# Optimization experiments

Measured on AMD Instinct MI355X. Metric: run time of the kernel, lower is better.

Reference implementation:

```python
import jax, jax.numpy as jnp
import numpy as np

B, C, H, W = 8, 768, 64, 64
BOT = 64   # bottleneck_dim
PD = 96    # prompt_dim
KP = 32    # number of prompt tokens
KK = 9     # 3x3 kernel points


def gelu(x):
    return jax.nn.gelu(x, approximate=False)  # torch nn.GELU default (erf)


def layernorm(x, g, b, eps=1e-5):
    m = jnp.mean(x, axis=-1, keepdims=True)
    v = jnp.var(x, axis=-1, keepdims=True)
    return (x - m) * jax.lax.rsqrt(v + eps) * g + b


def conv3x3(x, w, b):
    # x [B,Ci,H,W], w [Co,Ci,3,3] (torch layout), stride 1, pad 1
    y = jax.lax.conv_general_dilated(x, w, (1, 1), ((1, 1), (1, 1)))
    return y + b[None, :, None, None]


def deform_conv3x3(x, offset, w, pad=1):
    # mmcv DeformConv2d (v1, no mask, bias=False), deform_groups=1.
    # x [B,Ci,H,W]; offset [B,2*KK,H,W] in (dy,dx) pairs per kernel point.
    Bn, Ci, Hn, Wn = x.shape
    Co = w.shape[0]
    off = offset.reshape(Bn, KK, 2, Hn, Wn)
    dy, dx = off[:, :, 0], off[:, :, 1]                      # [B,KK,H,W]
    ky, kx = jnp.meshgrid(jnp.arange(3), jnp.arange(3), indexing='ij')
    py = (jnp.arange(Hn, dtype=x.dtype)[None, None, :, None] - pad
          + ky.reshape(1, KK, 1, 1).astype(x.dtype) + dy)    # sample rows
    px = (jnp.arange(Wn, dtype=x.dtype)[None, None, None, :] - pad
          + kx.reshape(1, KK, 1, 1).astype(x.dtype) + dx)    # sample cols
    y0 = jnp.floor(py)
    x0 = jnp.floor(px)
    wy = (py - y0)[:, None]                                   # [B,1,KK,H,W]
    wx = (px - x0)[:, None]
    xf = x.reshape(Bn, Ci, Hn * Wn)
    y0i = y0.astype(jnp.int32)
    x0i = x0.astype(jnp.int32)

    def samp(yi, xi):
        valid = ((yi >= 0) & (yi < Hn) & (xi >= 0) & (xi < Wn))
        yc = jnp.clip(yi, 0, Hn - 1)
        xc = jnp.clip(xi, 0, Wn - 1)
        idx = (yc * Wn + xc).reshape(Bn, -1)                  # [B,KK*H*W]
        g = jax.vmap(lambda f, i: f[:, i])(xf, idx)           # [B,Ci,KK*H*W]
        g = g.reshape(Bn, Ci, KK, Hn, Wn)
        return g * valid[:, None].astype(x.dtype)

    g00 = samp(y0i, x0i)
    g01 = samp(y0i, x0i + 1)
    g10 = samp(y0i + 1, x0i)
    g11 = samp(y0i + 1, x0i + 1)
    val = (g00 * (1 - wy) * (1 - wx) + g01 * (1 - wy) * wx
           + g10 * wy * (1 - wx) + g11 * wy * wx)             # [B,Ci,KK,H,W]
    return jnp.einsum('bckhw,ock->bohw', val, w.reshape(Co, Ci, KK))


def setup_inputs() -> dict:
    key = jax.random.key(0)
    ks = jax.random.split(key, 16)
    s = 0.02
    inp = {
        'x': jax.random.normal(ks[0], (B, C, H, W), jnp.float32),
        'irf': jax.random.normal(ks[1], (B, BOT, H, W), jnp.float32),
        'tf': jax.random.normal(ks[2], (KP, PD), jnp.float32),
        'ln_g': jnp.ones((C,), jnp.float32),
        'ln_b': jnp.zeros((C,), jnp.float32),
        'Wd': jax.random.normal(ks[3], (C, BOT), jnp.float32) * s,
        'bd': jnp.zeros((BOT,), jnp.float32),
        'Wu': jax.random.normal(ks[4], (BOT, C), jnp.float32) * s,
        'bu': jnp.zeros((C,), jnp.float32),
        'off_w': jax.random.normal(ks[5], (2 * KK, 2 * BOT, 3, 3), jnp.float32) * s,
        'off_b': jnp.zeros((2 * KK,), jnp.float32),
        'mod_w1': jax.random.normal(ks[6], (BOT // 4, BOT), jnp.float32) * s,
        'mod_b1': jnp.zeros((BOT // 4,), jnp.float32),
        'mod_w2': jax.random.normal(ks[7], (BOT, BOT // 4), jnp.float32) * s,
        'mod_b2': jnp.zeros((BOT,), jnp.float32),
        'dc_w': jax.random.normal(ks[8], (BOT, BOT, 3, 3), jnp.float32) * s,
        'alpha': jnp.full((1,), 0.1, jnp.float32),
        'Wk': jax.random.normal(ks[9], (PD, C), jnp.float32) * s,
        'bk': jnp.zeros((C,), jnp.float32),
        'Wv': jax.random.normal(ks[10], (PD, C), jnp.float32) * s,
        'bv': jnp.zeros((C,), jnp.float32),
        'temperature': jnp.full((1,), 0.07, jnp.float32),
        'Wg1': jax.random.normal(ks[11], (C, C // 4), jnp.float32) * s,
        'bg1': jnp.zeros((C // 4,), jnp.float32),
        'Wg2': jax.random.normal(ks[12], (C // 4, 1), jnp.float32) * s,
        'bg2': jnp.zeros((1,), jnp.float32),
        'scale': jnp.full((1,), 0.1, jnp.float32),
    }
    return inp


def reference(x, irf, tf, ln_g, ln_b, Wd, bd, Wu, bu, off_w, off_b,
              mod_w1, mod_b1, mod_w2, mod_b2, dc_w, alpha,
              Wk, bk, Wv, bv, temperature, Wg1, bg1, Wg2, bg2, scale):
    identity = x
    xp = jnp.transpose(x, (0, 2, 3, 1))                       # [B,H,W,C]
    x_down = gelu(layernorm(xp, ln_g, ln_b) @ Wd + bd)        # [B,H,W,BOT]
    # --- IRRGBFuse ---
    xc = jnp.transpose(x_down, (0, 3, 1, 2))                  # [B,BOT,H,W]
    offset = conv3x3(jnp.concatenate([xc, irf], axis=1), off_w, off_b)
    x_def = deform_conv3x3(xc, offset, dc_w)                  # [B,BOT,H,W]
    m = jnp.einsum('bchw,oc->bohw', irf, mod_w1) + mod_b1[None, :, None, None]
    m = jnp.einsum('bchw,oc->bohw', gelu(m), mod_w2) + mod_b2[None, :, None, None]
    m = jax.nn.sigmoid(m)
    x_fused = x_def + alpha * (x_def * m)
    x_fused = jnp.transpose(x_fused, (0, 2, 3, 1))            # [B,H,W,BOT]
    # --- up-projection + residual (dropout inactive in eval) ---
    x_up = x_fused @ Wu + bu
    x_res1 = xp + scale * x_up                                # [B,H,W,C]
    x_flat = x_res1.reshape(B, H * W, C)
    # --- cosine cross-attention over prompts ---
    pk = tf @ Wk + bk                                          # [K,C]
    pv = tf @ Wv + bv
    xn = x_flat / jnp.maximum(jnp.linalg.norm(x_flat, axis=-1, keepdims=True), 1e-12)
    pkn = pk / jnp.maximum(jnp.linalg.norm(pk, axis=-1, keepdims=True), 1e-12)
    cos = jnp.einsum('bnc,kc->bnk', xn, pkn)
    attn = jax.nn.softmax(cos / temperature, axis=-1)
    x_prompted = jnp.einsum('bnk,kc->bnc', attn, pv).reshape(B, H, W, C)
    # --- gate + residuals ---
    g = jax.nn.sigmoid(gelu(x_res1 @ Wg1 + bg1) @ Wg2 + bg2)   # [B,H,W,1]
    x_gated = x_res1 + g * x_prompted
    return identity + scale * jnp.transpose(x_gated, (0, 3, 1, 2))
```

## Files before the change

kernel.cpp:

```cpp
#include <hip/hip_runtime.h>
#include <hip/hip_bf16.h>
#include <math.h>

#define BN 8
#define C 768
#define H 64
#define W 64
#define HW 4096
#define BOT 64
#define PD 96
#define KP 32
#define KKN 9
#define NPX (BN*HW)

typedef __hip_bfloat16 bf16;
typedef __attribute__((ext_vector_type(8))) short bf16x8;
typedef __attribute__((ext_vector_type(4))) float f32x4;
#define MFMA16(a,b,c) __builtin_amdgcn_mfma_f32_16x16x32_bf16(a,b,c,0,0,0)

__device__ __forceinline__ float gelu_f(float x) {
    return 0.5f * x * (1.0f + erff(x * 0.70710678118654752440f));
}
__device__ __forceinline__ float sigmoid_f(float x) {
    return 1.0f / (1.0f + __expf(-x));
}
__device__ __forceinline__ float bf2f(short s) {
    return __uint_as_float(((unsigned)(unsigned short)s) << 16);
}

__global__ void k_prep(const float* __restrict__ Wd, const float* __restrict__ ln_g,
                       const float* __restrict__ ln_b, const float* __restrict__ bd,
                       const float* __restrict__ off_w, const float* __restrict__ dc_w,
                       const float* __restrict__ Wg1, const float* __restrict__ Wu,
                       const float* __restrict__ tf, const float* __restrict__ Wk,
                       const float* __restrict__ bk, const float* __restrict__ Wv,
                       const float* __restrict__ bv,
                       bf16* __restrict__ wdt, float* __restrict__ s12,
                       bf16* __restrict__ off_wt, bf16* __restrict__ dcb2,
                       bf16* __restrict__ wg1bt, bf16* __restrict__ wut,
                       float* __restrict__ pk, float* __restrict__ pvout) {
    int bx = blockIdx.x;
    int tid = threadIdx.x;
    if (bx < 192) {
        int i = bx*256 + tid;
        if (i < C*BOT) {
            int c = i >> 6, o = i & 63;
            wdt[(size_t)o*C + c] = __float2bfloat16(ln_g[c] * Wd[(size_t)c*BOT + o]);
        }
    } else if (bx == 192) {
        __shared__ float p1[4][64], p2[4][64];
        int o = tid & 63, part = tid >> 6;
        float a1 = 0.f, a2 = 0.f;
        for (int c = part; c < C; c += 4) {
            float wv = Wd[(size_t)c*BOT + o];
            a1 += ln_g[c] * wv;
            a2 += ln_b[c] * wv;
        }
        p1[part][o] = a1; p2[part][o] = a2;
        __syncthreads();
        if (tid < 64) {
            s12[o]      = p1[0][o]+p1[1][o]+p1[2][o]+p1[3][o];
            s12[64 + o] = p2[0][o]+p2[1][o]+p2[2][o]+p2[3][o] + bd[o];
        }
    } else if (bx < 337) {
        int i = (bx-193)*256 + tid;
        if (i < 32*1152) {
            int o = i / 1152, kk = i % 1152;
            int k = kk >> 7, ci = kk & 127;
            float v = (o < 18) ? off_w[(size_t)(o*128 + ci)*9 + k] : 0.0f;
            off_wt[i] = __float2bfloat16(v);
        }
    } else if (bx < 481) {
        int i = (bx-337)*256 + tid;
        if (i < 36864) {
            int e = i & 7;
            int lane = (i >> 3) & 63;
            int s = (i >> 9) & 1;
            int f = (i >> 10) & 3;
            int k = i >> 12;
            int lg = lane >> 4, lm = lane & 15;
            int o = f*16 + lm;
            int ci = s*32 + lg*8 + e;
            dcb2[i] = __float2bfloat16(dc_w[((size_t)o*64 + ci)*9 + k]);
        }
    } else if (bx < 1057) {
        int i = (bx-481)*256 + tid;
        if (i < 192*C) {
            int h = i / C, c = i % C;
            wg1bt[i] = __float2bfloat16(Wg1[(size_t)c*192 + h]);
        }
    } else if (bx < 1249) {
        int i = (bx-1057)*256 + tid;
        if (i < C*BOT) {
            int c = i >> 6, k = i & 63;
            wut[i] = __float2bfloat16(Wu[(size_t)k*C + c]);
        }
    } else {
        int i = (bx-1249)*256 + tid;
        if (i < KP*C) {
            int k = i / C, c = i % C;
            float aK = bk[c], aV = bv[c];
            for (int p = 0; p < PD; p++) {
                float tv = tf[k*PD+p];
                aK += tv * Wk[(size_t)p*C + c];
                aV += tv * Wv[(size_t)p*C + c];
            }
            pk[i] = aK; pvout[i] = aV;
        }
    }
}

__global__ void k_down_fused(const float* __restrict__ x, const bf16* __restrict__ wdt,
                             const float* __restrict__ s12, bf16* __restrict__ catb) {
    int gpix = blockIdx.x * 16;
    int b = gpix >> 12;
    int hw0 = gpix & 4095;
    int tid = threadIdx.x;
    int w = tid >> 6, lane = tid & 63;
    int lg = lane >> 4, lm = lane & 15;
    __shared__ float xt[2][64][18];
    const float* xb = x + (size_t)b*C*HW + hw0;
    int sc_ = tid >> 2;
    int sp  = (tid & 3) << 2;
    {
        float4 v = *(const float4*)(xb + (size_t)sc_*HW + sp);
        *(float2*)&xt[0][sc_][sp]     = make_float2(v.x, v.y);
        *(float2*)&xt[0][sc_][sp + 2] = make_float2(v.z, v.w);
    }
    __syncthreads();
    f32x4 acc0 = {0.f,0.f,0.f,0.f};
    float ssum = 0.f, sqsum = 0.f;
    const bf16* arow = wdt + (size_t)(w*16 + lm)*C;
    for (int kk = 0; kk < 12; kk++) {
        int cur = kk & 1;
        float4 nv;
        if (kk < 11)
            nv = *(const float4*)(xb + (size_t)((kk+1)*64 + sc_)*HW + sp);
#pragma unroll
        for (int s2 = 0; s2 < 2; s2++) {
            float xv[8];
#pragma unroll
            for (int e = 0; e < 8; e++) {
                float v = xt[cur][s2*32 + lg*8 + e][lm];
                xv[e] = v; ssum += v; sqsum += v*v;
            }
            union { bf16 h[8]; bf16x8 v; } ub;
#pragma unroll
            for (int e = 0; e < 8; e++) ub.h[e] = __float2bfloat16(xv[e]);
            bf16x8 a = *(const bf16x8*)(arow + kk*64 + s2*32 + lg*8);
            acc0 = MFMA16(a, ub.v, acc0);
        }
        if (kk < 11) {
            *(float2*)&xt[cur^1][sc_][sp]     = make_float2(nv.x, nv.y);
            *(float2*)&xt[cur^1][sc_][sp + 2] = make_float2(nv.z, nv.w);
        }
        __syncthreads();
    }
    ssum  += __shfl_xor(ssum, 16);  ssum  += __shfl_xor(ssum, 32);
    sqsum += __shfl_xor(sqsum, 16); sqsum += __shfl_xor(sqsum, 32);
    float mean = ssum * (1.0f/C);
    float var  = sqsum * (1.0f/C) - mean*mean;
    float rstd = rsqrtf(var + 1e-5f);
    bf16* dst = catb + (size_t)(gpix + lm)*128;
    union { bf16 h[4]; uint2 q; } u;
#pragma unroll
    for (int r = 0; r < 4; r++) {
        int o = w*16 + lg*4 + r;
        float y = rstd*(acc0[r] - mean*s12[o]) + s12[64 + o];
        u.h[r] = __float2bfloat16(gelu_f(y));
    }
    *(uint2*)(dst + w*16 + lg*4) = u.q;
}

__global__ void k_mod(const float* __restrict__ irf, const float* __restrict__ w1, const float* __restrict__ b1,
                      const float* __restrict__ w2, const float* __restrict__ b2,
                      bf16* __restrict__ mbf, bf16* __restrict__ catb) {
    int blk = blockIdx.x;
    int b = blk >> 6; int hw0 = (blk & 63)*64;
    int px = threadIdx.x & 63;
    int g = threadIdx.x >> 6;
    __shared__ float tile[64][64];
    __shared__ float hid[16][64];
    const float* ib = irf + (size_t)b*BOT*HW + hw0;
#pragma unroll
    for (int i = 0; i < 16; i++) {
        int ci = g + 4*i;
        tile[ci][px] = ib[(size_t)ci*HW + px];
    }
    __syncthreads();
    {
        int xp = threadIdx.x >> 2, q = threadIdx.x & 3;
        union { bf16 h[16]; uint4 v[2]; } u2;
#pragma unroll
        for (int i = 0; i < 16; i++) u2.h[i] = __float2bfloat16(tile[q*16 + i][xp]);
        uint4* d2 = (uint4*)(catb + (size_t)(b*HW + hw0 + xp)*128 + 64 + q*16);
        d2[0] = u2.v[0]; d2[1] = u2.v[1];
    }
#pragma unroll
    for (int jj = 0; jj < 4; jj++) {
        int j = g*4 + jj;
        float a = b1[j];
        for (int ci = 0; ci < 64; ci++) a += tile[ci][px] * w1[j*64+ci];
        hid[j][px] = gelu_f(a);
    }
    __syncthreads();
    union { bf16 h[16]; uint4 q[2]; } u;
#pragma unroll
    for (int s = 0; s < 16; s++) {
        int o = g*16 + s;
        float a = b2[o];
#pragma unroll
        for (int j = 0; j < 16; j++) a += hid[j][px] * w2[o*16+j];
        u.h[s] = __float2bfloat16(sigmoid_f(a));
    }
    uint4* dst = (uint4*)(mbf + (size_t)(b*HW + hw0 + px)*64 + g*16);
    dst[0] = u.q[0]; dst[1] = u.q[1];
}

__global__ void k_offconv_mfma(const bf16* __restrict__ catb, const bf16* __restrict__ off_wt,
                               const float* __restrict__ off_b, float* __restrict__ offs) {
    int blk = blockIdx.x;
    int b = blk >> 6, y = blk & 63;
    int tid = threadIdx.x;
    __shared__ uint4 lds4[3072];
    char* lds = (char*)lds4;
#pragma unroll
    for (int it = 0; it < 12; it++) {
        int idx = it*256 + tid;
        int ci8 = idx & 15, xx = (idx >> 4) & 63, lr = idx >> 10;
        int yy = y - 1 + lr;
        uint4 v = {0u,0u,0u,0u};
        if (yy >= 0 && yy < H)
            v = *(const uint4*)(catb + (size_t)(b*HW + yy*64 + xx)*128 + ci8*8);
        int lofs = (lr*16384 + xx*256) | ((ci8*16) ^ ((xx & 15) << 4));
        *(uint4*)(lds + lofs) = v;
    }
    __syncthreads();
    int w = tid >> 6, lane = tid & 63;
    int lg = lane >> 4, lm = lane & 15;
    f32x4 acc0 = {0.f,0.f,0.f,0.f}, acc1 = {0.f,0.f,0.f,0.f};
    const bf16* brow0 = off_wt + (size_t)lm*1152;
    const bf16* brow1 = off_wt + (size_t)(16+lm)*1152;
#pragma unroll
    for (int k = 0; k < 9; k++) {
        int ky = k/3, kx = k%3;
        int xs = w*16 + lm + kx - 1;
        bool valid = (xs >= 0 && xs < 64);
        int rowbase = ky*16384 + xs*256;
        int sw = (xs & 15) << 4;
#pragma unroll
        for (int ci0 = 0; ci0 < 128; ci0 += 32) {
            bf16x8 a = {0,0,0,0,0,0,0,0};
            if (valid) a = *(const bf16x8*)(lds + (rowbase | ((ci0*2 + lg*16) ^ sw)));
            bf16x8 bb0 = *(const bf16x8*)(brow0 + k*128 + ci0 + lg*8);
            bf16x8 bb1 = *(const bf16x8*)(brow1 + k*128 + ci0 + lg*8);
            acc0 = MFMA16(a, bb0, acc0);
            acc1 = MFMA16(a, bb1, acc1);
        }
    }
    float bi0 = off_b[lm];
    float bi1 = (lm < 2) ? off_b[16+lm] : 0.f;
#pragma unroll
    for (int r = 0; r < 4; r++) {
        int pr = w*16 + lg*4 + r;
        offs[(size_t)(b*18 + lm)*HW + y*64 + pr] = acc0[r] + bi0;
        if (lm < 2)
            offs[(size_t)(b*18 + 16 + lm)*HW + y*64 + pr] = acc1[r] + bi1;
    }
}

__global__ void k_deform_mfma(const bf16* __restrict__ catb, const float* __restrict__ offs,
                              const bf16* __restrict__ dcb2, const bf16* __restrict__ mbf,
                              const float* __restrict__ alpha, bf16* __restrict__ xfb) {
    int blk = blockIdx.x;
    int b = blk >> 6, y = blk & 63;
    int tid = threadIdx.x;
    __shared__ int   sy0[9][64];
    __shared__ int   sx0[9][64];
    __shared__ float swy[9][64];
    __shared__ float swx[9][64];
    for (int item = tid; item < 576; item += 256) {
        int k = item >> 6, xx = item & 63;
        float dy = offs[(size_t)(b*18 + 2*k  )*HW + y*W + xx];
        float dx = offs[(size_t)(b*18 + 2*k+1)*HW + y*W + xx];
        float py  = (float)(y  - 1 + k/3) + dy;
        float pxf = (float)(xx - 1 + k%3) + dx;
        float fy = floorf(py), fx = floorf(pxf);
        sy0[k][xx] = (int)fy;
        sx0[k][xx] = (int)fx;
        swy[k][xx] = py - fy;
        swx[k][xx] = pxf - fx;
    }
    __syncthreads();
    int w = tid >> 6, lane = tid & 63;
    int lg = lane >> 4, lm = lane & 15;
    int pix = w*16 + lm;
    const bf16* cb = catb + (size_t)b*HW*128;
    f32x4 acc[4];
#pragma unroll
    for (int f = 0; f < 4; f++) acc[f] = (f32x4){0.f,0.f,0.f,0.f};
#pragma unroll
    for (int k = 0; k < 9; k++) {
        int y0 = sy0[k][pix], x0 = sx0[k][pix];
        float wy = swy[k][pix], wx = swx[k][pix];
        bool vy0 = (y0 >= 0 && y0 < H), vy1 = (y0+1 >= 0 && y0+1 < H);
        bool vx0 = (x0 >= 0 && x0 < W), vx1 = (x0+1 >= 0 && x0+1 < W);
        float va[16];
#pragma unroll
        for (int i = 0; i < 16; i++) va[i] = 0.f;
#pragma unroll
        for (int cy = 0; cy < 2; cy++) {
#pragma unroll
            for (int cx = 0; cx < 2; cx++) {
                bool v = (cy ? vy1 : vy0) && (cx ? vx1 : vx0);
                if (v) {
                    float wc = (cy ? wy : (1.f-wy)) * (cx ? wx : (1.f-wx));
                    const bf16* base = cb + (size_t)((y0+cy)*64 + (x0+cx))*128;
                    bf16x8 v0 = *(const bf16x8*)(base + lg*8);
                    bf16x8 v1 = *(const bf16x8*)(base + 32 + lg*8);
#pragma unroll
                    for (int e = 0; e < 8; e++) {
                        va[e]   += wc * bf2f(v0[e]);
                        va[8+e] += wc * bf2f(v1[e]);
                    }
                }
            }
        }
        union { bf16 h[8]; bf16x8 v; } ua0, ua1;
#pragma unroll
        for (int e = 0; e < 8; e++) {
            ua0.h[e] = __float2bfloat16(va[e]);
            ua1.h[e] = __float2bfloat16(va[8+e]);
        }
        const bf16* dk = dcb2 + ((size_t)k*8*64 + lane)*8;
#pragma unroll
        for (int f = 0; f < 4; f++) {
            bf16x8 b0 = *(const bf16x8*)(dk + (size_t)(f*2+0)*64*8);
            bf16x8 b1 = *(const bf16x8*)(dk + (size_t)(f*2+1)*64*8);
            acc[f] = MFMA16(ua0.v, b0, acc[f]);
            acc[f] = MFMA16(ua1.v, b1, acc[f]);
        }
    }
    float al = alpha[0];
    const bf16* mrow = mbf + (size_t)(b*HW + y*64)*64;
    bf16* xrow = xfb + (size_t)(b*HW + y*64)*64;
    int prow = w*16 + lg*4;
#pragma unroll
    for (int f = 0; f < 4; f++) {
        int o = f*16 + lm;
#pragma unroll
        for (int r = 0; r < 4; r++) {
            int p = prow + r;
            float mm = __bfloat162float(mrow[(size_t)p*64 + o]);
            xrow[(size_t)p*64 + o] = __float2bfloat16(acc[f][r] * (1.f + al*mm));
        }
    }
}

__global__ void k_up_mfma(const float* __restrict__ x, const bf16* __restrict__ xfb,
                          const bf16* __restrict__ wut, const float* __restrict__ bu,
                          const float* __restrict__ scale, bf16* __restrict__ xres1) {
    int blk = blockIdx.x;
    int b = blk >> 6; int hw0 = (blk & 63)*64;
    int c00 = blockIdx.y * 192;
    int w = threadIdx.x >> 6, lane = threadIdx.x & 63;
    int lg = lane >> 4, lm = lane & 15;
    int prow = hw0 + w*16;
    const bf16* arow = xfb + (size_t)(b*HW + prow + lm)*BOT;
    bf16x8 a0 = *(const bf16x8*)(arow + lg*8);
    bf16x8 a1 = *(const bf16x8*)(arow + 32 + lg*8);
    float sc = scale[0];
    const float* xb = x + (size_t)b*C*HW;
    bf16* xrb = xres1 + (size_t)(b*HW)*C;
#pragma unroll 3
    for (int n0 = c00; n0 < c00 + 192; n0 += 64) {
        f32x4 acc[4];
#pragma unroll
        for (int f = 0; f < 4; f++) {
            int ncol = n0 + f*16 + lm;
            bf16x8 b0 = *(const bf16x8*)(wut + (size_t)ncol*BOT + lg*8);
            bf16x8 b1 = *(const bf16x8*)(wut + (size_t)ncol*BOT + 32 + lg*8);
            f32x4 t = {0.f,0.f,0.f,0.f};
            t = MFMA16(a0, b0, t);
            t = MFMA16(a1, b1, t);
            acc[f] = t;
        }
#pragma unroll
        for (int f = 0; f < 4; f++) {
            int c = n0 + f*16 + lm;
            float bias = bu[c];
#pragma unroll
            for (int r = 0; r < 4; r++) {
                int pix = prow + lg*4 + r;
                float xv = xb[(size_t)c*HW + pix];
                float rv = xv + sc*(acc[f][r] + bias);
                xrb[(size_t)pix*C + c] = __float2bfloat16(rv);
            }
        }
    }
}

__global__ void k_promptfin(const float* __restrict__ pk, const float* __restrict__ pv,
                            bf16* __restrict__ pkn, bf16* __restrict__ pvt) {
    if (blockIdx.x == 96) {
        __shared__ float part[32][9];
        __shared__ float rn[32];
        int t = threadIdx.x;
        int k = t >> 3, sl = t & 7;
        float s = 0.f;
        for (int c = sl; c < C; c += 8) { float v = pk[(size_t)k*C+c]; s += v*v; }
        part[k][sl] = s;
        __syncthreads();
        if (t < 32) {
            float tot = 0.f;
            for (int j = 0; j < 8; j++) tot += part[t][j];
            rn[t] = 1.0f / fmaxf(sqrtf(tot), 1e-12f);
        }
        __syncthreads();
        for (int i = t; i < KP*C; i += 256) pkn[i] = __float2bfloat16(pk[i] * rn[i/C]);
    } else {
        int i = blockIdx.x*256 + threadIdx.x;
        int c = i >> 5, k = i & 31;
        pvt[i] = __float2bfloat16(pv[(size_t)k*C + c]);
    }
}

__global__ void k_attn_gate(const bf16* __restrict__ xres1, const bf16* __restrict__ pkn,
                            const float* __restrict__ temp,
                            const bf16* __restrict__ wg1bt, const float* __restrict__ bg1,
                            const float* __restrict__ Wg2, const float* __restrict__ bg2,
                            bf16* __restrict__ atb, float* __restrict__ gbuf) {
    int pix0 = blockIdx.x * 32;
    int tid = threadIdx.x;
    int w = tid >> 6, lane = tid & 63;
    int lg = lane >> 4, lm = lane & 15;
    __shared__ char xt[32*1536];
    __shared__ float gl_part[2][32];

    {
        uint4 tmp[12];
#pragma unroll
        for (int it = 0; it < 12; it++) {
            int idx = it*256 + tid;
            int row = idx / 96, c16 = idx % 96;
            tmp[it] = *(const uint4*)(xres1 + (size_t)(pix0 + row)*C + c16*8);
        }
#pragma unroll
        for (int it = 0; it < 12; it++) {
            int idx = it*256 + tid;
            int row = idx / 96, c16 = idx % 96;
            int ofs = row*1536 + ((c16*16) ^ ((row & 7) << 4));
            *(uint4*)(xt + ofs) = tmp[it];
        }
    }
    __syncthreads();

    if (w < 2) {
        int prow = pix0 + w*16;
        int lrow = w*16 + lm;
        const char* arow = xt + lrow*1536;
        int sw = (lrow & 7) << 4;
        f32x4 acc0 = {0.f,0.f,0.f,0.f}, acc1 = {0.f,0.f,0.f,0.f};
        float ssq = 0.f;
        const bf16* b0row = pkn + (size_t)lm*C;
        const bf16* b1row = pkn + (size_t)(16 + lm)*C;
#pragma unroll 4
        for (int c0 = 0; c0 < C; c0 += 32) {
            bf16x8 a  = *(const bf16x8*)(arow + ((c0*2 + lg*16) ^ sw));
            bf16x8 b0 = *(const bf16x8*)(b0row + c0 + lg*8);
            bf16x8 b1 = *(const bf16x8*)(b1row + c0 + lg*8);
#pragma unroll
            for (int e = 0; e < 8; e++) {
                float av = bf2f(a[e]);
                ssq += av*av;
            }
            acc0 = MFMA16(a, b0, acc0);
            acc1 = MFMA16(a, b1, acc1);
        }
        ssq += __shfl_xor(ssq, 16);
        ssq += __shfl_xor(ssq, 32);
        float invnv = 1.0f / fmaxf(sqrtf(ssq), 1e-12f);
        float it = 1.0f / temp[0];
#pragma unroll
        for (int r = 0; r < 4; r++) {
            int pr = lg*4 + r;
            float iv = __shfl(invnv, pr);
            float s = iv * it;
            float v0 = acc0[r]*s, v1 = acc1[r]*s;
            float m = fmaxf(v0, v1);
            m = fmaxf(m, __shfl_xor(m, 1));
            m = fmaxf(m, __shfl_xor(m, 2));
            m = fmaxf(m, __shfl_xor(m, 4));
            m = fmaxf(m, __shfl_xor(m, 8));
            float e0 = __expf(v0-m), e1 = __expf(v1-m);
            float ss = e0 + e1;
            ss += __shfl_xor(ss, 1);
            ss += __shfl_xor(ss, 2);
            ss += __shfl_xor(ss, 4);
            ss += __shfl_xor(ss, 8);
            float inv = 1.0f / ss;
            bf16* ao = atb + (size_t)(prow + pr)*KP;
            ao[lm]      = __float2bfloat16(e0*inv);
            ao[16 + lm] = __float2bfloat16(e1*inv);
        }
    } else {
        int gw = w - 2;
        f32x4 acc[2][6];
#pragma unroll
        for (int pg = 0; pg < 2; pg++)
#pragma unroll
            for (int f = 0; f < 6; f++)
                acc[pg][f] = (f32x4){0.f,0.f,0.f,0.f};
        int lrow0 = lm, lrow1 = 16 + lm;
        const char* ar0 = xt + lrow0*1536;
        const char* ar1 = xt + lrow1*1536;
        int sw0 = (lrow0 & 7) << 4;
        int sw1 = (lrow1 & 7) << 4;
        const bf16* b0 = wg1bt + (size_t)(gw*96 + lm)*C;
        for (int c0 = 0; c0 < C; c0 += 32) {
            bf16x8 a[2], bb[6];
            a[0] = *(const bf16x8*)(ar0 + ((c0*2 + lg*16) ^ sw0));
            a[1] = *(const bf16x8*)(ar1 + ((c0*2 + lg*16) ^ sw1));
#pragma unroll
            for (int f = 0; f < 6; f++)
                bb[f] = *(const bf16x8*)(b0 + (size_t)f*16*C + c0 + lg*8);
#pragma unroll
            for (int pg = 0; pg < 2; pg++)
#pragma unroll
                for (int f = 0; f < 6; f++)
                    acc[pg][f] = MFMA16(a[pg], bb[f], acc[pg][f]);
        }
        float wg2v[6], bg1v[6];
#pragma unroll
        for (int f = 0; f < 6; f++) {
            int h = gw*96 + f*16 + lm;
            wg2v[f] = Wg2[h];
            bg1v[f] = bg1[h];
        }
#pragma unroll
        for (int pg = 0; pg < 2; pg++) {
#pragma unroll
            for (int r = 0; r < 4; r++) {
                float s = 0.f;
#pragma unroll
                for (int f = 0; f < 6; f++)
                    s += gelu_f(acc[pg][f][r] + bg1v[f]) * wg2v[f];
                s += __shfl_xor(s, 1);
                s += __shfl_xor(s, 2);
                s += __shfl_xor(s, 4);
                s += __shfl_xor(s, 8);
                if (lm == 0) gl_part[gw][pg*16 + lg*4 + r] = s;
            }
        }
    }
    __syncthreads();
    if (threadIdx.x < 32) {
        float t = gl_part[0][threadIdx.x] + gl_part[1][threadIdx.x];
        gbuf[pix0 + threadIdx.x] = sigmoid_f(t + bg2[0]);
    }
}

__global__ void k_out(const float* __restrict__ x, const bf16* __restrict__ xres1,
                      const bf16* __restrict__ atb, const float* __restrict__ gbuf,
                      const bf16* __restrict__ pvt, const float* __restrict__ scale,
                      float* __restrict__ out) {
    int blk = blockIdx.x;
    int pix0 = blk * 64;
    int b = blk >> 6; int hw0 = (blk & 63) * 64;
    int c0 = blockIdx.y * 192;
    int w = threadIdx.x >> 6, lane = threadIdx.x & 63;
    int lg = lane >> 4, lm = lane & 15;
    union { bf16 h[8]; bf16x8 v; } ua;
    ua.v = *(const bf16x8*)(atb + (size_t)(pix0 + w*16 + lm)*KP + lg*8);
    float sc = scale[0];
    float gv[4];
#pragma unroll
    for (int r = 0; r < 4; r++) gv[r] = gbuf[pix0 + w*16 + lg*4 + r];
    const float* xb = x + (size_t)b*C*HW;
    float* ob = out + (size_t)b*C*HW;
    int pbase = hw0 + w*16 + lg*4;
    const bf16* xr0 = xres1 + (size_t)(pix0 + w*16 + lg*4)*C;
#pragma unroll 3
    for (int n0 = c0; n0 < c0 + 192; n0 += 64) {
#pragma unroll
        for (int f = 0; f < 4; f++) {
            int c = n0 + f*16 + lm;
            bf16x8 bfrag = *(const bf16x8*)(pvt + (size_t)c*KP + lg*8);
            f32x4 z = {0.f,0.f,0.f,0.f};
            f32x4 acc = MFMA16(ua.v, bfrag, z);
            float4 x4 = *(const float4*)(xb + (size_t)c*HW + pbase);
            float4 o4;
            float xr;
            xr = __bfloat162float(xr0[c]);
            o4.x = x4.x + sc*(xr + gv[0]*acc[0]);
            xr = __bfloat162float(xr0[C + c]);
            o4.y = x4.y + sc*(xr + gv[1]*acc[1]);
            xr = __bfloat162float(xr0[2*C + c]);
            o4.z = x4.z + sc*(xr + gv[2]*acc[2]);
            xr = __bfloat162float(xr0[3*C + c]);
            o4.w = x4.w + sc*(xr + gv[3]*acc[3]);
            *(float4*)(ob + (size_t)c*HW + pbase) = o4;
        }
    }
}

extern "C" void kernel_launch(void* const* d_in, const int* in_sizes, int n_in,
                              void* d_out, int out_size, void* d_ws, size_t ws_size,
                              hipStream_t stream) {
    const float* x      = (const float*)d_in[0];
    const float* irf    = (const float*)d_in[1];
    const float* tf     = (const float*)d_in[2];
    const float* ln_g   = (const float*)d_in[3];
    const float* ln_b   = (const float*)d_in[4];
    const float* Wd     = (const float*)d_in[5];
    const float* bd     = (const float*)d_in[6];
    const float* Wu     = (const float*)d_in[7];
    const float* bu     = (const float*)d_in[8];
    const float* off_w  = (const float*)d_in[9];
    const float* off_b  = (const float*)d_in[10];
    const float* mod_w1 = (const float*)d_in[11];
    const float* mod_b1 = (const float*)d_in[12];
    const float* mod_w2 = (const float*)d_in[13];
    const float* mod_b2 = (const float*)d_in[14];
    const float* dc_w   = (const float*)d_in[15];
    const float* alpha  = (const float*)d_in[16];
    const float* Wk     = (const float*)d_in[17];
    const float* bk     = (const float*)d_in[18];
    const float* Wv     = (const float*)d_in[19];
    const float* bv     = (const float*)d_in[20];
    const float* temp   = (const float*)d_in[21];
    const float* Wg1    = (const float*)d_in[22];
    const float* bg1    = (const float*)d_in[23];
    const float* Wg2    = (const float*)d_in[24];
    const float* bg2    = (const float*)d_in[25];
    const float* scale  = (const float*)d_in[26];
    float* out = (float*)d_out;

    char* w = (char*)d_ws;
    auto alloc = [&](size_t bytes) {
        char* p = w;
        w += (bytes + 255) & ~(size_t)255;
        return p;
    };
    float* offs  = (float*)alloc((size_t)BN*18*HW*4);
    float* pk    = (float*)alloc((size_t)KP*C*4);
    float* pv    = (float*)alloc((size_t)KP*C*4);
    float* gbuf  = (float*)alloc((size_t)NPX*4);
    float* s12   = (float*)alloc((size_t)128*4);
    bf16* xres1  = (bf16*)alloc((size_t)NPX*C*2);
    bf16* pkn    = (bf16*)alloc((size_t)KP*C*2);
    bf16* pvt    = (bf16*)alloc((size_t)C*KP*2);
    bf16* atb    = (bf16*)alloc((size_t)NPX*KP*2);
    bf16* wg1bt  = (bf16*)alloc((size_t)192*C*2);
    bf16* catb   = (bf16*)alloc((size_t)NPX*128*2);
    bf16* offwt  = (bf16*)alloc((size_t)32*1152*2);
    bf16* xfb    = (bf16*)alloc((size_t)NPX*BOT*2);
    bf16* wut    = (bf16*)alloc((size_t)C*BOT*2);
    bf16* mbf    = (bf16*)alloc((size_t)NPX*BOT*2);
    bf16* dcb2   = (bf16*)alloc((size_t)36864*2);
    bf16* wdt    = (bf16*)alloc((size_t)C*BOT*2);

    k_prep<<<1345, 256, 0, stream>>>(Wd, ln_g, ln_b, bd, off_w, dc_w, Wg1, Wu,
                                     tf, Wk, bk, Wv, bv,
                                     wdt, s12, offwt, dcb2, wg1bt, wut, pk, pv);
    k_down_fused<<<2048, 256, 0, stream>>>(x, wdt, s12, catb);
    k_mod<<<512, 256, 0, stream>>>(irf, mod_w1, mod_b1, mod_w2, mod_b2, mbf, catb);
    k_offconv_mfma<<<512, 256, 0, stream>>>(catb, offwt, off_b, offs);
    k_deform_mfma<<<512, 256, 0, stream>>>(catb, offs, dcb2, mbf, alpha, xfb);
    k_up_mfma<<<dim3(512,4), 256, 0, stream>>>(x, xfb, wut, bu, scale, xres1);
    k_promptfin<<<97, 256, 0, stream>>>(pk, pv, pkn, pvt);
    k_attn_gate<<<1024, 256, 0, stream>>>(xres1, pkn, temp,
                                          wg1bt, bg1, Wg2, bg2, atb, gbuf);
    k_out<<<dim3(512,4), 256, 0, stream>>>(x, xres1, atb, gbuf, pvt, scale, out);
}
```

Measured before the change: 314.4 us.

## Widen down-projection tile to 64 pixels per block with per-wave pixel split

```diff
diff --git a/kernel.cpp b/kernel.cpp
--- a/kernel.cpp
+++ b/kernel.cpp
@@ -112,47 +112,63 @@
 
 __global__ void k_down_fused(const float* __restrict__ x, const bf16* __restrict__ wdt,
                              const float* __restrict__ s12, bf16* __restrict__ catb) {
-    int gpix = blockIdx.x * 16;
+    int gpix = blockIdx.x * 64;
     int b = gpix >> 12;
     int hw0 = gpix & 4095;
     int tid = threadIdx.x;
     int w = tid >> 6, lane = tid & 63;
     int lg = lane >> 4, lm = lane & 15;
-    __shared__ float xt[2][64][18];
+    __shared__ float xt[2][64][66];
     const float* xb = x + (size_t)b*C*HW + hw0;
-    int sc_ = tid >> 2;
-    int sp  = (tid & 3) << 2;
-    {
-        float4 v = *(const float4*)(xb + (size_t)sc_*HW + sp);
-        *(float2*)&xt[0][sc_][sp]     = make_float2(v.x, v.y);
-        *(float2*)&xt[0][sc_][sp + 2] = make_float2(v.z, v.w);
+    int cl  = w*16 + lg;
+    int pxl = (lane & 15) << 2;
+    float4 pre[4];
+#pragma unroll
+    for (int it = 0; it < 4; it++)
+        pre[it] = *(const float4*)(xb + (size_t)(cl + it*4)*HW + pxl);
+#pragma unroll
+    for (int it = 0; it < 4; it++) {
+        *(float2*)&xt[0][cl + it*4][pxl]     = make_float2(pre[it].x, pre[it].y);
+        *(float2*)&xt[0][cl + it*4][pxl + 2] = make_float2(pre[it].z, pre[it].w);
     }
     __syncthreads();
-    f32x4 acc0 = {0.f,0.f,0.f,0.f};
+    f32x4 acc[4];
+#pragma unroll
+    for (int f = 0; f < 4; f++) acc[f] = (f32x4){0.f,0.f,0.f,0.f};
     float ssum = 0.f, sqsum = 0.f;
-    const bf16* arow = wdt + (size_t)(w*16 + lm)*C;
+    int mypx = w*16 + lm;
     for (int kk = 0; kk < 12; kk++) {
         int cur = kk & 1;
-        float4 nv;
-        if (kk < 11)
-            nv = *(const float4*)(xb + (size_t)((kk+1)*64 + sc_)*HW + sp);
+        if (kk < 11) {
+#pragma unroll
+            for (int it = 0; it < 4; it++)
+                pre[it] = *(const float4*)(xb + (size_t)((kk+1)*64 + cl + it*4)*HW + pxl);
+        }
 #pragma unroll
         for (int s2 = 0; s2 < 2; s2++) {
             float xv[8];
 #pragma unroll
             for (int e = 0; e < 8; e++) {
-                float v = xt[cur][s2*32 + lg*8 + e][lm];
+                float v = xt[cur][s2*32 + lg*8 + e][mypx];
                 xv[e] = v; ssum += v; sqsum += v*v;
             }
             union { bf16 h[8]; bf16x8 v; } ub;
 #pragma unroll
             for (int e = 0; e < 8; e++) ub.h[e] = __float2bfloat16(xv[e]);
-            bf16x8 a = *(const bf16x8*)(arow + kk*64 + s2*32 + lg*8);
-            acc0 = MFMA16(a, ub.v, acc0);
+            int coff = kk*64 + s2*32 + lg*8;
+#pragma unroll
+            for (int of = 0; of < 4; of++) {
+                bf16x8 a = *(const bf16x8*)(wdt + (size_t)(of*16 + lm)*C + coff);
+                acc[of] = MFMA16(a, ub.v, acc[of]);
+            }
         }
         if (kk < 11) {
-            *(float2*)&xt[cur^1][sc_][sp]     = make_float2(nv.x, nv.y);
-            *(float2*)&xt[cur^1][sc_][sp + 2] = make_float2(nv.z, nv.w);
+            int nb = cur ^ 1;
+#pragma unroll
+            for (int it = 0; it < 4; it++) {
+                *(float2*)&xt[nb][cl + it*4][pxl]     = make_float2(pre[it].x, pre[it].y);
+                *(float2*)&xt[nb][cl + it*4][pxl + 2] = make_float2(pre[it].z, pre[it].w);
+            }
         }
         __syncthreads();
     }
@@ -161,15 +177,18 @@
     float mean = ssum * (1.0f/C);
     float var  = sqsum * (1.0f/C) - mean*mean;
     float rstd = rsqrtf(var + 1e-5f);
-    bf16* dst = catb + (size_t)(gpix + lm)*128;
-    union { bf16 h[4]; uint2 q; } u;
-#pragma unroll
-    for (int r = 0; r < 4; r++) {
-        int o = w*16 + lg*4 + r;
-        float y = rstd*(acc0[r] - mean*s12[o]) + s12[64 + o];
-        u.h[r] = __float2bfloat16(gelu_f(y));
-    }
-    *(uint2*)(dst + w*16 + lg*4) = u.q;
+    bf16* dst = catb + (size_t)(gpix + mypx)*128;
+#pragma unroll
+    for (int of = 0; of < 4; of++) {
+        union { bf16 h[4]; uint2 q; } u;
+#pragma unroll
+        for (int r = 0; r < 4; r++) {
+            int o = of*16 + lg*4 + r;
+            float y = rstd*(acc[of][r] - mean*s12[o]) + s12[64 + o];
+            u.h[r] = __float2bfloat16(gelu_f(y));
+        }
+        *(uint2*)(dst + of*16 + lg*4) = u.q;
+    }
 }
 
 __global__ void k_mod(const float* __restrict__ irf, const float* __restrict__ w1, const float* __restrict__ b1,
@@ -663,7 +682,7 @@
     k_prep<<<1345, 256, 0, stream>>>(Wd, ln_g, ln_b, bd, off_w, dc_w, Wg1, Wu,
                                      tf, Wk, bk, Wv, bv,
                                      wdt, s12, offwt, dcb2, wg1bt, wut, pk, pv);
-    k_down_fused<<<2048, 256, 0, stream>>>(x, wdt, s12, catb);
+    k_down_fused<<<512, 256, 0, stream>>>(x, wdt, s12, catb);
     k_mod<<<512, 256, 0, stream>>>(irf, mod_w1, mod_b1, mod_w2, mod_b2, mbf, catb);
     k_offconv_mfma<<<512, 256, 0, stream>>>(catb, offwt, off_b, offs);
     k_deform_mfma<<<512, 256, 0, stream>>>(catb, offs, dcb2, mbf, alpha, xfb);
```

Result: no change. 316.1 us (+0.6%).
